# Kernel optimization log

Measured on AMD Instinct MI355X. Metric: run time of the kernel, lower is better.

Reference implementation:

```python
import jax, jax.numpy as jnp
import numpy as np

T, B, I, H, O = 1024, 512, 32, 256, 32

def setup_inputs() -> dict:
    key = jax.random.key(0)
    ks = jax.random.split(key, 8)
    s_ih = 1.0 / np.sqrt(H)
    return {
        "input_states": jax.random.normal(ks[0], (T, B, I), jnp.float32),
        "physical_predictions": jax.random.normal(ks[1], (T, B, O), jnp.float32),
        "W_ih": jax.random.uniform(ks[2], (4 * H, I), jnp.float32, -s_ih, s_ih),
        "W_hh": jax.random.uniform(ks[3], (4 * H, H), jnp.float32, -s_ih, s_ih),
        "b_ih": jax.random.uniform(ks[4], (4 * H,), jnp.float32, -s_ih, s_ih),
        "b_hh": jax.random.uniform(ks[5], (4 * H,), jnp.float32, -s_ih, s_ih),
        "W_out": jax.random.uniform(ks[6], (O, H), jnp.float32, -s_ih, s_ih),
        "b_out": jax.random.uniform(ks[7], (O,), jnp.float32, -s_ih, s_ih),
    }

def reference(input_states, physical_predictions, W_ih, W_hh, b_ih, b_hh, W_out, b_out):
    # Teacher-forced LSTM rollout (teacher_force_probability=0 -> always use input_sequence[t]),
    # use_physics_as_bias=1 -> full_pred = physical_predictions[t] + linear(h_t).
    Bsz = input_states.shape[1]
    Hd = W_hh.shape[1]
    dt = input_states.dtype

    def step(carry, xs):
        h, c = carry
        x, phys = xs                                   # [B,I], [B,O]
        gates = x @ W_ih.T + b_ih + h @ W_hh.T + b_hh  # [B,4H]
        i_g, f_g, g_g, o_g = jnp.split(gates, 4, axis=-1)
        i_g = jax.nn.sigmoid(i_g)
        f_g = jax.nn.sigmoid(f_g)
        g_g = jnp.tanh(g_g)
        o_g = jax.nn.sigmoid(o_g)
        c = f_g * c + i_g * g_g
        h = o_g * jnp.tanh(c)
        rnn_pred = h @ W_out.T + b_out                 # [B,O]
        full_pred = phys + rnn_pred
        return (h, c), (full_pred, rnn_pred)

    h0 = jnp.zeros((Bsz, Hd), dt)
    c0 = jnp.zeros((Bsz, Hd), dt)
    _, (full_preds, rnn_preds) = jax.lax.scan(step, (h0, c0), (input_states, physical_predictions))
    # torch.stack(preds, 1) -> [B, T, O]
    return jnp.transpose(full_preds, (1, 0, 2)), jnp.transpose(rnn_preds, (1, 0, 2))
```

## Files before the change

kernel.cpp:

```cpp
#include <hip/hip_runtime.h>
#include <hip/hip_bf16.h>
#include <stdint.h>

typedef unsigned short u16;
typedef unsigned char  u8;
typedef unsigned int   u32;
typedef unsigned long long u64;
typedef __attribute__((ext_vector_type(8))) _Float16 f16x8;
typedef __attribute__((ext_vector_type(4))) float f32x4;

#define TSTEPS 1024
#define BATCH  512
#define INDIM  32
#define HID    256
#define ODIM   32
#define NCH    66
#define KCH    9

#define WS_BC (NCH*KCH*64*8*2)
#define WS_XP (WS_BC + 4096)
#define WS_XS (WS_XP + 32*2*8*128*8)

#define MFMA(a,b,c) __builtin_amdgcn_mfma_f32_16x16x32_f16((a),(b),(c),0,0,0)
#define AGL(p)   __hip_atomic_load((p),      __ATOMIC_RELAXED, __HIP_MEMORY_SCOPE_AGENT)
#define AGS(p,v) __hip_atomic_store((p),(v), __ATOMIC_RELAXED, __HIP_MEMORY_SCOPE_AGENT)

__device__ __forceinline__ u16 f2h(float v){ _Float16 h=(_Float16)v; return *(u16*)&h; }
__device__ __forceinline__ float sigf(float x){ return 1.0f/(1.0f+__expf(-x)); }
__device__ __forceinline__ float tanhf_(float x){
    float ax=fabsf(x); float e=__expf(-2.f*ax); float t=(1.f-e)/(1.f+e); return copysignf(t,x);
}
__device__ __forceinline__ f16x8 cvt8(float4 a, float4 b){
    f16x8 r;
    r[0]=(_Float16)a.x; r[1]=(_Float16)a.y; r[2]=(_Float16)a.z; r[3]=(_Float16)a.w;
    r[4]=(_Float16)b.x; r[5]=(_Float16)b.y; r[6]=(_Float16)b.z; r[7]=(_Float16)b.w;
    return r;
}

__device__ __forceinline__ void ld4_sc0(const u8* p, uint4& a, uint4& b, uint4& c, uint4& d){
    asm volatile(
        "global_load_dwordx4 %0, %4, off sc0\n\t"
        "global_load_dwordx4 %1, %4, off offset:1024 sc0\n\t"
        "global_load_dwordx4 %2, %4, off offset:2048 sc0\n\t"
        "global_load_dwordx4 %3, %4, off offset:3072 sc0\n\t"
        "s_waitcnt vmcnt(0)"
        : "=&v"(a), "=&v"(b), "=&v"(c), "=&v"(d)
        : "v"(p) : "memory");
    __builtin_amdgcn_sched_barrier(0);
}
__device__ __forceinline__ void st_u64_sc0(u64* p, u64 v){
    asm volatile("global_store_dwordx2 %0, %1, off sc0" :: "v"(p), "v"(v) : "memory");
}

__global__ __launch_bounds__(256) void prepack_kernel(
    const float* __restrict__ W_ih, const float* __restrict__ W_hh,
    const float* __restrict__ b_ih, const float* __restrict__ b_hh,
    const float* __restrict__ W_out,
    u16* __restrict__ Wb, float* __restrict__ Bc)
{
    int tid = blockIdx.x*blockDim.x + threadIdx.x;
    int stride = gridDim.x*blockDim.x;
    const int TOT = NCH*KCH*64*8;
    for (int idx = tid; idx < TOT; idx += stride) {
        int j    = idx & 7;
        int lane = (idx >> 3) & 63;
        int ck   = idx >> 9;
        int kc   = ck % KCH;
        int c    = ck / KCH;
        int kl   = ((lane >> 4) << 3) + j;
        float v;
        if (c < 64) {
            int g = c >> 4;
            int m = (c & 15) * 16 + (lane & 15);
            if (kc < 8) v = W_hh[(g*HID + m)*HID + (kc*32 + kl)];
            else        v = W_ih[(g*HID + m)*INDIM + kl];
        } else {
            int o = ((c - 64) << 4) + (lane & 15);
            v = (kc < 8) ? W_out[o*HID + kc*32 + kl] : 0.f;
        }
        Wb[idx] = f2h(v);
    }
    for (int n = tid; n < 1024; n += stride) {
        int c = n >> 4, qq = n & 15;
        int g = c >> 4;
        int m = (c & 15) * 16 + qq;
        Bc[n] = b_ih[g*HID + m] + b_hh[g*HID + m];
    }
}

__global__ __launch_bounds__(256) void init_xbuf_kernel(u64* __restrict__ xp, u64* __restrict__ xs) {
    int i = blockIdx.x*256 + threadIdx.x;
    AGS(xp + i, 1ull);
    AGS(xs + i, 1ull);
}

__global__ __launch_bounds__(64, 1) void lstm_kernel(
    const float* __restrict__ xin,
    const float* __restrict__ phys,
    const u16*  __restrict__ Wb_,
    const float* __restrict__ Bc,
    const float* __restrict__ b_out,
    u64* __restrict__ xp,
    u64* __restrict__ xs,
    float* __restrict__ out)
{
    const int lane = threadIdx.x;
    const int bid  = blockIdx.x;
    const int tile = bid & 31;
    const int ug   = bid >> 5;
    const int b0   = tile << 4;
    const int q    = lane & 15;
    const int rg   = lane >> 4;
    const int mrb  = rg << 2;

    __shared__ u16 scr[256];

    const f16x8* Wb8 = (const f16x8*)Wb_;

    f16x8 wg0[KCH], wg1[KCH], wg2[KCH], wg3[KCH];
#pragma unroll
    for (int kc = 0; kc < KCH; ++kc) {
        wg0[kc] = Wb8[((0*16+ug)*KCH + kc)*64 + lane];
        wg1[kc] = Wb8[((1*16+ug)*KCH + kc)*64 + lane];
        wg2[kc] = Wb8[((2*16+ug)*KCH + kc)*64 + lane];
        wg3[kc] = Wb8[((3*16+ug)*KCH + kc)*64 + lane];
    }
    f16x8 wp[8];
#pragma unroll
    for (int kc = 0; kc < 8; ++kc)
        wp[kc] = Wb8[((64 + (ug>>3))*KCH + kc)*64 + lane];

    const float bi0 = Bc[((0*16+ug)<<4)+q];
    const float bi1 = Bc[((1*16+ug)<<4)+q];
    const float bi2 = Bc[((2*16+ug)<<4)+q];
    const float bi3 = Bc[((3*16+ug)<<4)+q];

    const bool  isP = (ug == 0) || (ug == 8);
    const int   o_  = ((ug >> 3) << 4) + q;
    const float bip = isP ? b_out[o_] : 0.f;

    float ph0=0.f, ph1=0.f, ph2=0.f, ph3=0.f;
    if (isP) {
        ph0 = phys[(size_t)(b0+mrb+0)*ODIM + o_];
        ph1 = phys[(size_t)(b0+mrb+1)*ODIM + o_];
        ph2 = phys[(size_t)(b0+mrb+2)*ODIM + o_];
        ph3 = phys[(size_t)(b0+mrb+3)*ODIM + o_];
    }

    const float* xbase = xin + (size_t)(b0 + q)*INDIM + (rg << 3);
    float4 xc0 = *(const float4*)(xbase);
    float4 xc1 = *(const float4*)(xbase + 4);
    float4 xn0 = *(const float4*)(xbase + (size_t)BATCH*INDIM);
    float4 xn1 = *(const float4*)(xbase + (size_t)BATCH*INDIM + 4);

    const int m_ = (lane>>1) & 15, s_ = lane>>5, c_ = lane & 1;
    const int gw = ((m_ + 16*(((ug&1)<<1) + s_)) << 1) + c_;
    const int kcSelf = ug >> 1;
    u64* xpT = xp + (size_t)tile*2048;
    u64* xsT = xs + (size_t)tile*2048;

    float* outFull = out;
    float* outRnn  = out + (size_t)BATCH*TSTEPS*ODIM;

    float cs0=0.f, cs1=0.f, cs2=0.f, cs3=0.f;
    f16x8 h0,h1,h2,h3,h4,h5,h6,h7;
    bool fastm = true;

    for (int t = 0; t < TSTEPS; ++t) {
        f32x4 a0={bi0,bi0,bi0,bi0}, a1={bi1,bi1,bi1,bi1};
        f32x4 a2={bi2,bi2,bi2,bi2}, a3={bi3,bi3,bi3,bi3};
        {
            f16x8 ax = cvt8(xc0, xc1);
            a0=MFMA(ax,wg0[8],a0); a1=MFMA(ax,wg1[8],a1);
            a2=MFMA(ax,wg2[8],a2); a3=MFMA(ax,wg3[8],a3);
        }

        if (t > 0) {
            const u8*  pb = (const u8*)xpT + (size_t)(t&1)*8192 + lane*16;
            const u64* sb = xsT + (size_t)(t&1)*1024 + lane*2;
            const u32  gx = (u32)(((t-1) >> 1) & 1);
            union U { uint4 u; f16x8 h; u64 qq[2]; } A,B,C,D,E,F,G,H;
            int iter = 0;
            for (;;) {
                if (fastm) {
                    ld4_sc0(pb,        A.u,B.u,C.u,D.u);
                    ld4_sc0(pb + 4096, E.u,F.u,G.u,H.u);
                } else {
                    A.qq[0]=AGL(sb+0*128); A.qq[1]=AGL(sb+0*128+1);
                    B.qq[0]=AGL(sb+1*128); B.qq[1]=AGL(sb+1*128+1);
                    C.qq[0]=AGL(sb+2*128); C.qq[1]=AGL(sb+2*128+1);
                    D.qq[0]=AGL(sb+3*128); D.qq[1]=AGL(sb+3*128+1);
                    E.qq[0]=AGL(sb+4*128); E.qq[1]=AGL(sb+4*128+1);
                    F.qq[0]=AGL(sb+5*128); F.qq[1]=AGL(sb+5*128+1);
                    G.qq[0]=AGL(sb+6*128); G.qq[1]=AGL(sb+6*128+1);
                    H.qq[0]=AGL(sb+7*128); H.qq[1]=AGL(sb+7*128+1);
                }
                u32 bad = ((A.u.x^gx)|(A.u.z^gx)|(B.u.x^gx)|(B.u.z^gx)
                          |(C.u.x^gx)|(C.u.z^gx)|(D.u.x^gx)|(D.u.z^gx)
                          |(E.u.x^gx)|(E.u.z^gx)|(F.u.x^gx)|(F.u.z^gx)
                          |(G.u.x^gx)|(G.u.z^gx)|(H.u.x^gx)|(H.u.z^gx)) & 1u;
                if (!__any((int)bad)) { h0=A.h;h1=B.h;h2=C.h;h3=D.h;h4=E.h;h5=F.h;h6=G.h;h7=H.h; break; }
                if (fastm && ++iter >= 256) fastm = false;
            }

            a0=MFMA(h0,wg0[0],a0); a1=MFMA(h0,wg1[0],a1); a2=MFMA(h0,wg2[0],a2); a3=MFMA(h0,wg3[0],a3);
            a0=MFMA(h1,wg0[1],a0); a1=MFMA(h1,wg1[1],a1); a2=MFMA(h1,wg2[1],a2); a3=MFMA(h1,wg3[1],a3);
            a0=MFMA(h2,wg0[2],a0); a1=MFMA(h2,wg1[2],a1); a2=MFMA(h2,wg2[2],a2); a3=MFMA(h2,wg3[2],a3);
            a0=MFMA(h3,wg0[3],a0); a1=MFMA(h3,wg1[3],a1); a2=MFMA(h3,wg2[3],a2); a3=MFMA(h3,wg3[3],a3);
            a0=MFMA(h4,wg0[4],a0); a1=MFMA(h4,wg1[4],a1); a2=MFMA(h4,wg2[4],a2); a3=MFMA(h4,wg3[4],a3);
            a0=MFMA(h5,wg0[5],a0); a1=MFMA(h5,wg1[5],a1); a2=MFMA(h5,wg2[5],a2); a3=MFMA(h5,wg3[5],a3);
            a0=MFMA(h6,wg0[6],a0); a1=MFMA(h6,wg1[6],a1); a2=MFMA(h6,wg2[6],a2); a3=MFMA(h6,wg3[6],a3);
            a0=MFMA(h7,wg0[7],a0); a1=MFMA(h7,wg1[7],a1); a2=MFMA(h7,wg2[7],a2); a3=MFMA(h7,wg3[7],a3);
        }

        {
            float gi,gf,gg,go,hv;
            gi=sigf(a0[0]); gf=sigf(a1[0]); gg=tanhf_(a2[0]); go=sigf(a3[0]);
            cs0 = gf*cs0 + gi*gg; hv = go*tanhf_(cs0);
            scr[(mrb+0 + 16*(q>>3))*8 + (q&7)] = f2h(hv);
            gi=sigf(a0[1]); gf=sigf(a1[1]); gg=tanhf_(a2[1]); go=sigf(a3[1]);
            cs1 = gf*cs1 + gi*gg; hv = go*tanhf_(cs1);
            scr[(mrb+1 + 16*(q>>3))*8 + (q&7)] = f2h(hv);
            gi=sigf(a0[2]); gf=sigf(a1[2]); gg=tanhf_(a2[2]); go=sigf(a3[2]);
            cs2 = gf*cs2 + gi*gg; hv = go*tanhf_(cs2);
            scr[(mrb+2 + 16*(q>>3))*8 + (q&7)] = f2h(hv);
            gi=sigf(a0[3]); gf=sigf(a1[3]); gg=tanhf_(a2[3]); go=sigf(a3[3]);
            cs3 = gf*cs3 + gi*gg; hv = go*tanhf_(cs3);
            scr[(mrb+3 + 16*(q>>3))*8 + (q&7)] = f2h(hv);

            u16 w0b=scr[lane*4+0], w1b=scr[lane*4+1], w2b=scr[lane*4+2], w3b=scr[lane*4+3];
            u64 pub = (u64)w0b | ((u64)w1b<<16) | ((u64)w2b<<32) | ((u64)w3b<<48);
            pub = (pub & ~1ull) | (u64)((t>>1)&1);
            const size_t off = (size_t)((t+1)&1)*1024 + kcSelf*128 + gw;
            st_u64_sc0(xpT + off, pub);
            AGS(xsT + off, pub);
        }

        if (isP && t > 0) {
            f32x4 pa = {bip,bip,bip,bip};
            pa=MFMA(h0,wp[0],pa); pa=MFMA(h1,wp[1],pa);
            pa=MFMA(h2,wp[2],pa); pa=MFMA(h3,wp[3],pa);
            pa=MFMA(h4,wp[4],pa); pa=MFMA(h5,wp[5],pa);
            pa=MFMA(h6,wp[6],pa); pa=MFMA(h7,wp[7],pa);
            const size_t ob = (size_t)(b0+mrb)*TSTEPS*ODIM + (size_t)(t-1)*ODIM + o_;
            const size_t rs = (size_t)TSTEPS*ODIM;
            outFull[ob+0*rs] = ph0 + pa[0];  outRnn[ob+0*rs] = pa[0];
            outFull[ob+1*rs] = ph1 + pa[1];  outRnn[ob+1*rs] = pa[1];
            outFull[ob+2*rs] = ph2 + pa[2];  outRnn[ob+2*rs] = pa[2];
            outFull[ob+3*rs] = ph3 + pa[3];  outRnn[ob+3*rs] = pa[3];
            const float* pb2 = phys + (size_t)t*BATCH*ODIM + (size_t)(b0+mrb)*ODIM + o_;
            ph0 = pb2[0*ODIM]; ph1 = pb2[1*ODIM]; ph2 = pb2[2*ODIM]; ph3 = pb2[3*ODIM];
        }

        {
            int tt = (t+2 < TSTEPS) ? (t+2) : (TSTEPS-1);
            const float* p = xbase + (size_t)tt*BATCH*INDIM;
            float4 nn0 = *(const float4*)p;
            float4 nn1 = *(const float4*)(p + 4);
            xc0 = xn0; xc1 = xn1; xn0 = nn0; xn1 = nn1;
        }
    }

    if (isP) {
        const u8*  pb = (const u8*)xpT + lane*16;
        const u64* sb = xsT + lane*2;
        union U { uint4 u; f16x8 h; u64 qq[2]; } A,B,C,D,E,F,G,H;
        int iter = 0;
        for (;;) {
            if (fastm) {
                ld4_sc0(pb,        A.u,B.u,C.u,D.u);
                ld4_sc0(pb + 4096, E.u,F.u,G.u,H.u);
            } else {
                A.qq[0]=AGL(sb+0*128); A.qq[1]=AGL(sb+0*128+1);
                B.qq[0]=AGL(sb+1*128); B.qq[1]=AGL(sb+1*128+1);
                C.qq[0]=AGL(sb+2*128); C.qq[1]=AGL(sb+2*128+1);
                D.qq[0]=AGL(sb+3*128); D.qq[1]=AGL(sb+3*128+1);
                E.qq[0]=AGL(sb+4*128); E.qq[1]=AGL(sb+4*128+1);
                F.qq[0]=AGL(sb+5*128); F.qq[1]=AGL(sb+5*128+1);
                G.qq[0]=AGL(sb+6*128); G.qq[1]=AGL(sb+6*128+1);
                H.qq[0]=AGL(sb+7*128); H.qq[1]=AGL(sb+7*128+1);
            }
            u32 bad = ((A.u.x^1u)|(A.u.z^1u)|(B.u.x^1u)|(B.u.z^1u)
                      |(C.u.x^1u)|(C.u.z^1u)|(D.u.x^1u)|(D.u.z^1u)
                      |(E.u.x^1u)|(E.u.z^1u)|(F.u.x^1u)|(F.u.z^1u)
                      |(G.u.x^1u)|(G.u.z^1u)|(H.u.x^1u)|(H.u.z^1u)) & 1u;
            if (!__any((int)bad)) { h0=A.h;h1=B.h;h2=C.h;h3=D.h;h4=E.h;h5=F.h;h6=G.h;h7=H.h; break; }
            if (fastm && ++iter >= 256) fastm = false;
        }
        f32x4 pa = {bip,bip,bip,bip};
        pa=MFMA(h0,wp[0],pa); pa=MFMA(h1,wp[1],pa);
        pa=MFMA(h2,wp[2],pa); pa=MFMA(h3,wp[3],pa);
        pa=MFMA(h4,wp[4],pa); pa=MFMA(h5,wp[5],pa);
        pa=MFMA(h6,wp[6],pa); pa=MFMA(h7,wp[7],pa);
        const size_t ob = (size_t)(b0+mrb)*TSTEPS*ODIM + (size_t)1023*ODIM + o_;
        const size_t rs = (size_t)TSTEPS*ODIM;
        outFull[ob+0*rs] = ph0 + pa[0];  outRnn[ob+0*rs] = pa[0];
        outFull[ob+1*rs] = ph1 + pa[1];  outRnn[ob+1*rs] = pa[1];
        outFull[ob+2*rs] = ph2 + pa[2];  outRnn[ob+2*rs] = pa[2];
        outFull[ob+3*rs] = ph3 + pa[3];  outRnn[ob+3*rs] = pa[3];
    }
}

extern "C" void kernel_launch(void* const* d_in, const int* in_sizes, int n_in,
                              void* d_out, int out_size, void* d_ws, size_t ws_size,
                              hipStream_t stream) {
    const float* xin   = (const float*)d_in[0];
    const float* phys  = (const float*)d_in[1];
    const float* W_ih  = (const float*)d_in[2];
    const float* W_hh  = (const float*)d_in[3];
    const float* b_ih  = (const float*)d_in[4];
    const float* b_hh  = (const float*)d_in[5];
    const float* W_out = (const float*)d_in[6];
    const float* b_out = (const float*)d_in[7];

    char*  ws = (char*)d_ws;
    u16*   Wb = (u16*)ws;
    float* Bc = (float*)(ws + WS_BC);
    u64*   xp = (u64*)(ws + WS_XP);
    u64*   xs = (u64*)(ws + WS_XS);

    prepack_kernel<<<256, 256, 0, stream>>>(W_ih, W_hh, b_ih, b_hh, W_out, Wb, Bc);
    init_xbuf_kernel<<<256, 256, 0, stream>>>(xp, xs);
    lstm_kernel<<<512, 64, 0, stream>>>(xin, phys, Wb, Bc, b_out, xp, xs, (float*)d_out);
}
```

Measured before the change: 2.214 ms.

## Rotate output projection across eight blocks and merge h polling loads

The per-step output projection and its stores, which used to fall on the two blocks with ug 0 and 8, now rotate among the eight blocks per output half, selected by ug&7 matching (t-1)&7. Each block prefetches its phys values seven steps ahead, so the critical-path blocks no longer do projection work every step. The two 4-load polling batches are merged into one 8-load batch with a single wait, and the x input conversion and prefetch move before the h-dependent MFMAs. The fast-poll fallback threshold is also raised from 256 to 4096 iterations.

```diff
diff --git a/kernel.cpp b/kernel.cpp
--- a/kernel.cpp
+++ b/kernel.cpp
@@ -37,15 +37,20 @@
     return r;
 }
 
-__device__ __forceinline__ void ld4_sc0(const u8* p, uint4& a, uint4& b, uint4& c, uint4& d){
+__device__ __forceinline__ void ld8_sc0(const u8* p0, const u8* p1,
+    uint4& a, uint4& b, uint4& c, uint4& d, uint4& e, uint4& f, uint4& g, uint4& h){
     asm volatile(
-        "global_load_dwordx4 %0, %4, off sc0\n\t"
-        "global_load_dwordx4 %1, %4, off offset:1024 sc0\n\t"
-        "global_load_dwordx4 %2, %4, off offset:2048 sc0\n\t"
-        "global_load_dwordx4 %3, %4, off offset:3072 sc0\n\t"
+        "global_load_dwordx4 %0, %8, off sc0\n\t"
+        "global_load_dwordx4 %1, %8, off offset:1024 sc0\n\t"
+        "global_load_dwordx4 %2, %8, off offset:2048 sc0\n\t"
+        "global_load_dwordx4 %3, %8, off offset:3072 sc0\n\t"
+        "global_load_dwordx4 %4, %9, off sc0\n\t"
+        "global_load_dwordx4 %5, %9, off offset:1024 sc0\n\t"
+        "global_load_dwordx4 %6, %9, off offset:2048 sc0\n\t"
+        "global_load_dwordx4 %7, %9, off offset:3072 sc0\n\t"
         "s_waitcnt vmcnt(0)"
-        : "=&v"(a), "=&v"(b), "=&v"(c), "=&v"(d)
-        : "v"(p) : "memory");
+        : "=&v"(a), "=&v"(b), "=&v"(c), "=&v"(d), "=&v"(e), "=&v"(f), "=&v"(g), "=&v"(h)
+        : "v"(p0), "v"(p1) : "memory");
     __builtin_amdgcn_sched_barrier(0);
 }
 __device__ __forceinline__ void st_u64_sc0(u64* p, u64 v){
@@ -112,6 +117,7 @@
     const int q    = lane & 15;
     const int rg   = lane >> 4;
     const int mrb  = rg << 2;
+    const int k8   = ug & 7;
 
     __shared__ u16 scr[256];
 
@@ -135,23 +141,25 @@
     const float bi2 = Bc[((2*16+ug)<<4)+q];
     const float bi3 = Bc[((3*16+ug)<<4)+q];
 
-    const bool  isP = (ug == 0) || (ug == 8);
     const int   o_  = ((ug >> 3) << 4) + q;
-    const float bip = isP ? b_out[o_] : 0.f;
-
-    float ph0=0.f, ph1=0.f, ph2=0.f, ph3=0.f;
-    if (isP) {
-        ph0 = phys[(size_t)(b0+mrb+0)*ODIM + o_];
-        ph1 = phys[(size_t)(b0+mrb+1)*ODIM + o_];
-        ph2 = phys[(size_t)(b0+mrb+2)*ODIM + o_];
-        ph3 = phys[(size_t)(b0+mrb+3)*ODIM + o_];
+    const float bip = b_out[o_];
+
+    float ph0, ph1, ph2, ph3;
+    {
+        const float* pb = phys + (size_t)k8*BATCH*ODIM + (size_t)(b0+mrb)*ODIM + o_;
+        ph0 = pb[0*ODIM]; ph1 = pb[1*ODIM]; ph2 = pb[2*ODIM]; ph3 = pb[3*ODIM];
     }
 
     const float* xbase = xin + (size_t)(b0 + q)*INDIM + (rg << 3);
-    float4 xc0 = *(const float4*)(xbase);
-    float4 xc1 = *(const float4*)(xbase + 4);
-    float4 xn0 = *(const float4*)(xbase + (size_t)BATCH*INDIM);
-    float4 xn1 = *(const float4*)(xbase + (size_t)BATCH*INDIM + 4);
+    f16x8 axc;
+    float4 xn0, xn1;
+    {
+        float4 c0 = *(const float4*)(xbase);
+        float4 c1 = *(const float4*)(xbase + 4);
+        axc = cvt8(c0, c1);
+        xn0 = *(const float4*)(xbase + (size_t)BATCH*INDIM);
+        xn1 = *(const float4*)(xbase + (size_t)BATCH*INDIM + 4);
+    }
 
     const int m_ = (lane>>1) & 15, s_ = lane>>5, c_ = lane & 1;
     const int gw = ((m_ + 16*(((ug&1)<<1) + s_)) << 1) + c_;
@@ -169,22 +177,19 @@
     for (int t = 0; t < TSTEPS; ++t) {
         f32x4 a0={bi0,bi0,bi0,bi0}, a1={bi1,bi1,bi1,bi1};
         f32x4 a2={bi2,bi2,bi2,bi2}, a3={bi3,bi3,bi3,bi3};
-        {
-            f16x8 ax = cvt8(xc0, xc1);
-            a0=MFMA(ax,wg0[8],a0); a1=MFMA(ax,wg1[8],a1);
-            a2=MFMA(ax,wg2[8],a2); a3=MFMA(ax,wg3[8],a3);
-        }
+        a0=MFMA(axc,wg0[8],a0); a1=MFMA(axc,wg1[8],a1);
+        a2=MFMA(axc,wg2[8],a2); a3=MFMA(axc,wg3[8],a3);
 
         if (t > 0) {
-            const u8*  pb = (const u8*)xpT + (size_t)(t&1)*8192 + lane*16;
-            const u64* sb = xsT + (size_t)(t&1)*1024 + lane*2;
-            const u32  gx = (u32)(((t-1) >> 1) & 1);
+            const u8*  pb0 = (const u8*)xpT + (size_t)(t&1)*8192 + lane*16;
+            const u8*  pb1 = pb0 + 4096;
+            const u64* sb  = xsT + (size_t)(t&1)*1024 + lane*2;
+            const u32  gx  = (u32)(((t-1) >> 1) & 1);
             union U { uint4 u; f16x8 h; u64 qq[2]; } A,B,C,D,E,F,G,H;
             int iter = 0;
             for (;;) {
                 if (fastm) {
-                    ld4_sc0(pb,        A.u,B.u,C.u,D.u);
-                    ld4_sc0(pb + 4096, E.u,F.u,G.u,H.u);
+                    ld8_sc0(pb0, pb1, A.u,B.u,C.u,D.u,E.u,F.u,G.u,H.u);
                 } else {
                     A.qq[0]=AGL(sb+0*128); A.qq[1]=AGL(sb+0*128+1);
                     B.qq[0]=AGL(sb+1*128); B.qq[1]=AGL(sb+1*128+1);
@@ -200,9 +205,19 @@
                           |(E.u.x^gx)|(E.u.z^gx)|(F.u.x^gx)|(F.u.z^gx)
                           |(G.u.x^gx)|(G.u.z^gx)|(H.u.x^gx)|(H.u.z^gx)) & 1u;
                 if (!__any((int)bad)) { h0=A.h;h1=B.h;h2=C.h;h3=D.h;h4=E.h;h5=F.h;h6=G.h;h7=H.h; break; }
-                if (fastm && ++iter >= 256) fastm = false;
+                if (fastm && ++iter >= 4096) fastm = false;
             }
-
+        }
+
+        {
+            axc = cvt8(xn0, xn1);
+            int tt = (t+2 < TSTEPS) ? (t+2) : (TSTEPS-1);
+            const float* p = xbase + (size_t)tt*BATCH*INDIM;
+            xn0 = *(const float4*)p;
+            xn1 = *(const float4*)(p + 4);
+        }
+
+        if (t > 0) {
             a0=MFMA(h0,wg0[0],a0); a1=MFMA(h0,wg1[0],a1); a2=MFMA(h0,wg2[0],a2); a3=MFMA(h0,wg3[0],a3);
             a0=MFMA(h1,wg0[1],a0); a1=MFMA(h1,wg1[1],a1); a2=MFMA(h1,wg2[1],a2); a3=MFMA(h1,wg3[1],a3);
             a0=MFMA(h2,wg0[2],a0); a1=MFMA(h2,wg1[2],a1); a2=MFMA(h2,wg2[2],a2); a3=MFMA(h2,wg3[2],a3);
@@ -236,7 +251,7 @@
             AGS(xsT + off, pub);
         }
 
-        if (isP && t > 0) {
+        if (t > 0 && k8 == ((t-1) & 7)) {
             f32x4 pa = {bip,bip,bip,bip};
             pa=MFMA(h0,wp[0],pa); pa=MFMA(h1,wp[1],pa);
             pa=MFMA(h2,wp[2],pa); pa=MFMA(h3,wp[3],pa);
@@ -248,28 +263,21 @@
             outFull[ob+1*rs] = ph1 + pa[1];  outRnn[ob+1*rs] = pa[1];
             outFull[ob+2*rs] = ph2 + pa[2];  outRnn[ob+2*rs] = pa[2];
             outFull[ob+3*rs] = ph3 + pa[3];  outRnn[ob+3*rs] = pa[3];
-            const float* pb2 = phys + (size_t)t*BATCH*ODIM + (size_t)(b0+mrb)*ODIM + o_;
-            ph0 = pb2[0*ODIM]; ph1 = pb2[1*ODIM]; ph2 = pb2[2*ODIM]; ph3 = pb2[3*ODIM];
-        }
-
-        {
-            int tt = (t+2 < TSTEPS) ? (t+2) : (TSTEPS-1);
-            const float* p = xbase + (size_t)tt*BATCH*INDIM;
-            float4 nn0 = *(const float4*)p;
-            float4 nn1 = *(const float4*)(p + 4);
-            xc0 = xn0; xc1 = xn1; xn0 = nn0; xn1 = nn1;
-        }
-    }
-
-    if (isP) {
-        const u8*  pb = (const u8*)xpT + lane*16;
-        const u64* sb = xsT + lane*2;
+            int tn = (t + 7 <= TSTEPS-1) ? (t + 7) : (TSTEPS-1);
+            const float* pb = phys + (size_t)tn*BATCH*ODIM + (size_t)(b0+mrb)*ODIM + o_;
+            ph0 = pb[0*ODIM]; ph1 = pb[1*ODIM]; ph2 = pb[2*ODIM]; ph3 = pb[3*ODIM];
+        }
+    }
+
+    if (k8 == 7) {
+        const u8*  pb0 = (const u8*)xpT + lane*16;
+        const u8*  pb1 = pb0 + 4096;
+        const u64* sb  = xsT + lane*2;
         union U { uint4 u; f16x8 h; u64 qq[2]; } A,B,C,D,E,F,G,H;
         int iter = 0;
         for (;;) {
             if (fastm) {
-                ld4_sc0(pb,        A.u,B.u,C.u,D.u);
-                ld4_sc0(pb + 4096, E.u,F.u,G.u,H.u);
+                ld8_sc0(pb0, pb1, A.u,B.u,C.u,D.u,E.u,F.u,G.u,H.u);
             } else {
                 A.qq[0]=AGL(sb+0*128); A.qq[1]=AGL(sb+0*128+1);
                 B.qq[0]=AGL(sb+1*128); B.qq[1]=AGL(sb+1*128+1);
@@ -285,7 +293,7 @@
                       |(E.u.x^1u)|(E.u.z^1u)|(F.u.x^1u)|(F.u.z^1u)
                       |(G.u.x^1u)|(G.u.z^1u)|(H.u.x^1u)|(H.u.z^1u)) & 1u;
             if (!__any((int)bad)) { h0=A.h;h1=B.h;h2=C.h;h3=D.h;h4=E.h;h5=F.h;h6=G.h;h7=H.h; break; }
-            if (fastm && ++iter >= 256) fastm = false;
+            if (fastm && ++iter >= 4096) fastm = false;
         }
         f32x4 pa = {bip,bip,bip,bip};
         pa=MFMA(h0,wp[0],pa); pa=MFMA(h1,wp[1],pa);
```

Measured after the change: 3.006 ms. 35.8% more time.
